# Kernel optimization log

Measured on AMD Instinct MI355X. Metric: run time of the kernel, lower is better.

## Reference

```python
import jax, jax.numpy as jnp
import numpy as np

B, S, H = 4, 2048, 768
NUM_POS = B * (S // 4)  # fixed count of positive clc_label entries (2048, even)
NEG_BIG = -1000000000.0


def setup_inputs() -> dict:
    key = jax.random.key(0)
    k1, k2, k3, k4, k5 = jax.random.split(key, 5)
    encoded_states = jax.random.normal(k1, (B, S, H), dtype=jnp.float32)
    # sorted cell-ids -> contiguous segments for the equality mask
    indicator = jnp.sort(jax.random.randint(k2, (B, S), 0, 256, dtype=jnp.int32), axis=-1)
    # clc_label: first S//4 positions per row are positive targets (class ids in [1,S)),
    # last S//2 positions are -1 (attendable keys), rest 0 (ignored)
    pos_labels = jax.random.randint(k3, (B, S // 4), 1, S, dtype=jnp.int32)
    clc_label = jnp.zeros((B, S), dtype=jnp.int32)
    clc_label = clc_label.at[:, : S // 4].set(pos_labels)
    clc_label = clc_label.at[:, S // 2:].set(-1)
    # uniform_linear params (torch Linear: y = x @ W.T + b)
    W = jax.random.normal(k4, (H, H), dtype=jnp.float32) / np.sqrt(H)
    b = jax.random.normal(k5, (H,), dtype=jnp.float32) * 0.01
    return {"encoded_states": encoded_states, "W": W, "b": b,
            "indicator": indicator, "clc_label": clc_label}


def _ce(logits, labels):
    # mean cross entropy; all labels are > 0 here so ignore_index=0 never triggers
    logp = jax.nn.log_softmax(logits, axis=-1)
    return -jnp.take_along_axis(logp, labels[:, None], axis=1).mean()


def reference(encoded_states, W, b, indicator, clc_label):
    # indicator-equality mask matmul == within-segment sum (the segment-reduce emulation)
    seg_mask = (indicator[:, :, None] == indicator[:, None, :]).astype(encoded_states.dtype)  # [B,S,S]
    agg = jnp.einsum("bij,bjh->bih", seg_mask, encoded_states)  # [B,S,H]
    # Q and K use the SAME linear on the same input -> compute once
    proj = jnp.tanh(agg @ W.T + b)  # [B,S,H]
    scores = jnp.einsum("bih,bjh->bij", proj, proj)  # [B,S,S]
    # attend only to positions where clc_label < 0
    allow = (clc_label < 0)[:, None, :]  # [B,1,S]
    scores = scores + jnp.where(allow, 0.0, NEG_BIG).astype(scores.dtype)
    flat = scores.reshape(-1, S)          # [B*S, S]
    labels = clc_label.reshape(-1)        # [B*S]
    pos_idx = jnp.nonzero(labels > 0, size=NUM_POS)[0]  # row-major order == torch bool-indexing
    logits = flat[pos_idx]                # [NUM_POS, S]
    labs = labels[pos_idx]                # [NUM_POS]
    sep_logits, sep_labels = logits[0::2], labs[0::2]
    tok_logits, tok_labels = logits[1::2], labs[1::2]
    sep_loss = _ce(sep_logits, sep_labels)
    tok_loss = _ce(tok_logits, tok_labels)
    sep_correct = jnp.sum((jnp.argmax(sep_logits, axis=-1).astype(jnp.int32) == sep_labels).astype(jnp.float32))
    tok_correct = jnp.sum((jnp.argmax(tok_logits, axis=-1).astype(jnp.int32) == tok_labels).astype(jnp.float32))
    sep_count = jnp.asarray(sep_logits.shape[0] + 1e-6, dtype=jnp.float32)
    tok_count = jnp.asarray(tok_logits.shape[0] + 1e-6, dtype=jnp.float32)
    return ((sep_loss, sep_correct, sep_count), (tok_loss, tok_correct, tok_count))
```

## Files before the change

### kernel.cpp

```cpp
#include <hip/hip_runtime.h>
#include <math.h>
#include <limits.h>

#define BB 4
#define SS 2048
#define HH 768
#define MAXSEG 256
#define NUM_POS (BB*(SS/4))
#define NEG_BIG -1000000000.0f
#define NSEGSUM (BB*MAXSEG)
#define NWCAST  576

typedef _Float16 f16x8 __attribute__((ext_vector_type(8)));
typedef _Float16 f16x4 __attribute__((ext_vector_type(4)));
typedef float    f32x4 __attribute__((ext_vector_type(4)));

__device__ __forceinline__ int blockExclScan(int v, int* sWave, int lane, int wid)
{
  int x = v;
  #pragma unroll
  for (int off = 1; off < 64; off <<= 1) {
    int y = __shfl_up(x, off, 64);
    if (lane >= off) x += y;
  }
  if (lane == 63) sWave[wid] = x;
  __syncthreads();
  int base = 0;
  for (int w = 0; w < wid; w++) base += sWave[w];
  return base + x - v;
}

__global__ __launch_bounds__(256) void k_front(
    const float* __restrict__ es, const float* __restrict__ W,
    const int* __restrict__ ind, const int* __restrict__ clc,
    _Float16* __restrict__ segsum_h, _Float16* __restrict__ Wh,
    int* __restrict__ seg_id, int* __restrict__ pos_cnt,
    int* __restrict__ allowCnt, int* __restrict__ firstAllow,
    int* __restrict__ posSegOff, int* __restrict__ posSeg,
    float* __restrict__ accum, int* __restrict__ counter)
{
  int t = threadIdx.x;
  int lane = t & 63, wid = t >> 6;
  int blk = blockIdx.x;

  __shared__ int sInd[SS];
  __shared__ int sWave[4];
  __shared__ int sAC[MAXSEG];
  __shared__ int sFA[MAXSEG];
  __shared__ int sStEn[2];

  if (blk >= NSEGSUM + BB) {
    int idx = (blk - NSEGSUM - BB)*256 + t;
    float4 v = ((const float4*)W)[idx];
    f16x4 h;
    h[0] = (_Float16)v.x; h[1] = (_Float16)v.y;
    h[2] = (_Float16)v.z; h[3] = (_Float16)v.w;
    *(f16x4*)(Wh + (size_t)idx*4) = h;
    return;
  }

  if (blk < NSEGSUM) {
    int b = blk >> 8, s = blk & 255;
    for (int i = t; i < SS; i += 256) sInd[i] = ind[b*SS + i];
    if (t == 0) { sStEn[0] = SS; sStEn[1] = SS; }
    __syncthreads();
    int i0 = t * 8;
    int f[8]; int lsum = 0;
    #pragma unroll
    for (int u = 0; u < 8; u++) {
      int i = i0 + u;
      f[u] = (i == 0) ? 0 : (sInd[i] != sInd[i-1]);
      lsum += f[u];
    }
    int run = blockExclScan(lsum, sWave, lane, wid);
    #pragma unroll
    for (int u = 0; u < 8; u++) {
      int i = i0 + u;
      run += f[u];
      if (run == s   && (f[u] || i == 0)) sStEn[0] = i;
      if (run == s+1 && f[u])             sStEn[1] = i;
    }
    __syncthreads();
    int st = sStEn[0], en = sStEn[1];
    float4 acc = {0.f, 0.f, 0.f, 0.f};
    if (t < 192 && st < SS) {
      const float* basep = es + (size_t)b*SS*HH + t*4;
      for (int i = st; i < en; i++) {
        float4 v = *(const float4*)(basep + (size_t)i*HH);
        acc.x += v.x; acc.y += v.y; acc.z += v.z; acc.w += v.w;
      }
    }
    if (t < 192) {
      f16x4 h;
      h[0] = (_Float16)acc.x; h[1] = (_Float16)acc.y;
      h[2] = (_Float16)acc.z; h[3] = (_Float16)acc.w;
      *(f16x4*)(segsum_h + ((size_t)b*MAXSEG + s)*HH + t*4) = h;
    }
    return;
  }

  int b = blk - NSEGSUM;
  if (b == 0 && t < 4) accum[t] = 0.f;
  if (b == 0 && t == 4) *counter = 0;
  for (int i = t; i < SS; i += 256) sInd[i] = ind[b*SS + i];
  sAC[t] = 0; sFA[t] = INT_MAX;
  __syncthreads();

  int i0 = t * 8;
  int f[8], cv[8];
  int lsum = 0;
  #pragma unroll
  for (int u = 0; u < 8; u++) {
    int i = i0 + u;
    f[u] = (i == 0) ? 0 : (sInd[i] != sInd[i-1]);
    cv[u] = clc[b*SS + i];
    lsum += f[u];
  }
  int run = blockExclScan(lsum, sWave, lane, wid);
  int rid[8];
  #pragma unroll
  for (int u = 0; u < 8; u++) {
    run += f[u];
    rid[u] = run;
    seg_id[b*SS + i0 + u] = run;
  }

  #pragma unroll
  for (int u = 0; u < 8; u++) {
    if (cv[u] < 0) {
      atomicAdd(&sAC[rid[u]], 1);
      atomicMin(&sFA[rid[u]], i0 + u);
    }
  }
  __syncthreads();
  allowCnt[b*MAXSEG + t]   = sAC[t];
  firstAllow[b*MAXSEG + t] = sFA[t];
  __syncthreads();

  int p[8], kk[8];
  int psum = 0;
  #pragma unroll
  for (int u = 0; u < 8; u++) { p[u] = (cv[u] > 0) ? 1 : 0; psum += p[u]; }
  int rank = blockExclScan(psum, sWave, lane, wid);
  #pragma unroll
  for (int u = 0; u < 8; u++) {
    kk[u] = rank;
    if (p[u]) rank++;
  }
  if (t == 255) pos_cnt[b] = rank;
  __syncthreads();

  sAC[t] = 0;
  __syncthreads();
  #pragma unroll
  for (int u = 0; u < 8; u++) if (p[u]) atomicAdd(&sAC[rid[u]], 1);
  __syncthreads();
  int cnt = sAC[t];
  int off = blockExclScan(cnt, sWave, lane, wid);
  posSegOff[b*(MAXSEG+1) + t] = off;
  if (t == 255) posSegOff[b*(MAXSEG+1) + 256] = off + cnt;
  __syncthreads();
  sFA[t] = off;
  __syncthreads();
  #pragma unroll
  for (int u = 0; u < 8; u++) {
    if (p[u]) {
      int pos = atomicAdd(&sFA[rid[u]], 1);
      posSeg[b*SS + pos] = (kk[u] << 16) | (i0 + u);
    }
  }
}

__global__ __launch_bounds__(256) void k_gemmU(
    const _Float16* __restrict__ Ah, const _Float16* __restrict__ Wh,
    const float* __restrict__ bias, _Float16* __restrict__ Uh)
{
  int tid = threadIdx.x;
  int w = tid >> 6, lane = tid & 63;
  int tile = blockIdx.x*4 + w;
  int tm = tile / 24, tn = tile % 24;
  int rb = tm*32, cb = tn*32;
  int m0 = lane & 15, quad = lane >> 4;
  const _Float16* A0 = Ah + (size_t)(rb + m0)*HH + quad*8;
  const _Float16* A1 = A0 + (size_t)16*HH;
  const _Float16* B0 = Wh + (size_t)(cb + m0)*HH + quad*8;
  const _Float16* B1 = B0 + (size_t)16*HH;
  f32x4 acc00 = {0.f,0.f,0.f,0.f}, acc01 = {0.f,0.f,0.f,0.f};
  f32x4 acc10 = {0.f,0.f,0.f,0.f}, acc11 = {0.f,0.f,0.f,0.f};
  #pragma unroll 4
  for (int k0 = 0; k0 < HH; k0 += 32) {
    f16x8 a0 = *(const f16x8*)(A0 + k0);
    f16x8 a1 = *(const f16x8*)(A1 + k0);
    f16x8 b0 = *(const f16x8*)(B0 + k0);
    f16x8 b1 = *(const f16x8*)(B1 + k0);
    acc00 = __builtin_amdgcn_mfma_f32_16x16x32_f16(a0, b0, acc00, 0, 0, 0);
    acc01 = __builtin_amdgcn_mfma_f32_16x16x32_f16(a0, b1, acc01, 0, 0, 0);
    acc10 = __builtin_amdgcn_mfma_f32_16x16x32_f16(a1, b0, acc10, 0, 0, 0);
    acc11 = __builtin_amdgcn_mfma_f32_16x16x32_f16(a1, b1, acc11, 0, 0, 0);
  }
  float bc0 = bias[cb + m0], bc1 = bias[cb + 16 + m0];
  int r0 = rb + quad*4;
  #pragma unroll
  for (int i = 0; i < 4; i++) {
    Uh[(size_t)(r0+i)*HH    + cb + m0]      = (_Float16)tanhf(acc00[i] + bc0);
    Uh[(size_t)(r0+i)*HH    + cb + 16 + m0] = (_Float16)tanhf(acc01[i] + bc1);
    Uh[(size_t)(r0+16+i)*HH + cb + m0]      = (_Float16)tanhf(acc10[i] + bc0);
    Uh[(size_t)(r0+16+i)*HH + cb + 16 + m0] = (_Float16)tanhf(acc11[i] + bc1);
  }
}

__global__ __launch_bounds__(256) void k_gramtail(
    const _Float16* __restrict__ Uh, const int* __restrict__ seg_id,
    const int* __restrict__ clc, const int* __restrict__ pos_cnt,
    const int* __restrict__ allowCnt, const int* __restrict__ firstAllow,
    const int* __restrict__ posSegOff, const int* __restrict__ posSeg,
    float* __restrict__ accum, int* __restrict__ counter,
    float* __restrict__ out)
{
  __shared__ float Gs[16][260];
  __shared__ float sP[4][4];
  int t = threadIdx.x;
  int lane = t & 63, wid = t >> 6;
  int b = blockIdx.x >> 4;
  int rb = (blockIdx.x & 15) * 16;
  int m0 = lane & 15, quad = lane >> 4;
  const _Float16* Ub = Uh + (size_t)b*MAXSEG*HH;
  const _Float16* Ap = Ub + (size_t)(rb + m0)*HH + quad*8;

  #pragma unroll
  for (int ct = 0; ct < 4; ct++) {
    int cb = (wid*4 + ct)*16;
    const _Float16* Bp = Ub + (size_t)(cb + m0)*HH + quad*8;
    f32x4 acc = {0.f,0.f,0.f,0.f};
    #pragma unroll 4
    for (int k0 = 0; k0 < HH; k0 += 32) {
      f16x8 a  = *(const f16x8*)(Ap + k0);
      f16x8 bb = *(const f16x8*)(Bp + k0);
      acc = __builtin_amdgcn_mfma_f32_16x16x32_f16(a, bb, acc, 0, 0, 0);
    }
    #pragma unroll
    for (int i = 0; i < 4; i++)
      Gs[quad*4 + i][cb + m0] = acc[i];
  }
  __syncthreads();

  const int* ac = allowCnt + b*MAXSEG;
  const int* fa = firstAllow + b*MAXSEG;
  int base_b = 0;
  for (int x = 0; x < b; x++) base_b += pos_cnt[x];
  float l0 = 0.f, c0 = 0.f, l1 = 0.f, c1 = 0.f;

  #pragma unroll
  for (int q2 = 0; q2 < 4; q2++) {
    int row = wid*4 + q2;
    int si = rb + row;
    float gv[4]; int av[4], fv[4];
    #pragma unroll
    for (int q = 0; q < 4; q++) {
      int s2 = lane + 64*q;
      gv[q] = Gs[row][s2]; av[q] = ac[s2]; fv[q] = fa[s2];
    }
    float m = -INFINITY;
    #pragma unroll
    for (int q = 0; q < 4; q++) if (av[q] > 0) m = fmaxf(m, gv[q]);
    #pragma unroll
    for (int off = 32; off > 0; off >>= 1) m = fmaxf(m, __shfl_xor(m, off, 64));
    float s = 0.f;
    #pragma unroll
    for (int q = 0; q < 4; q++) if (av[q] > 0) s += (float)av[q] * expf(gv[q] - m);
    #pragma unroll
    for (int off = 32; off > 0; off >>= 1) s += __shfl_xor(s, off, 64);
    float bv = -INFINITY; int bi = INT_MAX;
    #pragma unroll
    for (int q = 0; q < 4; q++) {
      if (av[q] > 0 && (gv[q] > bv || (gv[q] == bv && fv[q] < bi))) { bv = gv[q]; bi = fv[q]; }
    }
    #pragma unroll
    for (int off = 32; off > 0; off >>= 1) {
      float ov = __shfl_xor(bv, off, 64);
      int   oi = __shfl_xor(bi, off, 64);
      if (ov > bv || (ov == bv && oi < bi)) { bv = ov; bi = oi; }
    }
    float lseV = m + logf(s);

    int st = posSegOff[b*(MAXSEG+1) + si];
    int en = posSegOff[b*(MAXSEG+1) + si + 1];
    for (int pp = st + lane; pp < en; pp += 64) {
      int e = posSeg[b*SS + pp];
      int i = e & 0xFFFF, k = e >> 16;
      int L = clc[b*SS + i];
      int sL = seg_id[b*SS + L];
      float vL = Gs[row][sL] + (clc[b*SS + L] < 0 ? 0.0f : NEG_BIG);
      float loss = lseV - vL;
      float corr = (bi == L) ? 1.0f : 0.0f;
      if ((base_b + k) & 1) { l1 += loss; c1 += corr; }
      else                  { l0 += loss; c0 += corr; }
    }
  }

  #pragma unroll
  for (int off = 32; off > 0; off >>= 1) {
    l0 += __shfl_down(l0, off, 64);
    c0 += __shfl_down(c0, off, 64);
    l1 += __shfl_down(l1, off, 64);
    c1 += __shfl_down(c1, off, 64);
  }
  if (lane == 0) { sP[wid][0] = l0; sP[wid][1] = c0; sP[wid][2] = l1; sP[wid][3] = c1; }
  __syncthreads();
  if (t == 0) {
    atomicAdd(&accum[0], sP[0][0]+sP[1][0]+sP[2][0]+sP[3][0]);
    atomicAdd(&accum[1], sP[0][1]+sP[1][1]+sP[2][1]+sP[3][1]);
    atomicAdd(&accum[2], sP[0][2]+sP[1][2]+sP[2][2]+sP[3][2]);
    atomicAdd(&accum[3], sP[0][3]+sP[1][3]+sP[2][3]+sP[3][3]);
    __threadfence();
    int old = atomicAdd(counter, 1);
    if (old == (int)gridDim.x - 1) {
      float L0 = atomicAdd(&accum[0], 0.0f);
      float C0 = atomicAdd(&accum[1], 0.0f);
      float L1 = atomicAdd(&accum[2], 0.0f);
      float C1 = atomicAdd(&accum[3], 0.0f);
      float n = (float)(NUM_POS/2);
      out[0] = L0 / n;
      out[1] = C0;
      out[2] = n + 1e-6f;
      out[3] = L1 / n;
      out[4] = C1;
      out[5] = n + 1e-6f;
    }
  }
}

extern "C" void kernel_launch(void* const* d_in, const int* in_sizes, int n_in,
                              void* d_out, int out_size, void* d_ws, size_t ws_size,
                              hipStream_t stream)
{
  const float* es   = (const float*)d_in[0];
  const float* W    = (const float*)d_in[1];
  const float* bias = (const float*)d_in[2];
  const int*   ind  = (const int*)d_in[3];
  const int*   clc  = (const int*)d_in[4];
  float* out = (float*)d_out;

  char* ws = (char*)d_ws;
  float* accum      = (float*)(ws + 0);
  int*   counter    = (int*)(ws + 16);
  int*   pos_cnt    = (int*)(ws + 512);
  int*   seg_id     = (int*)(ws + 8192);
  int*   posSegOff  = (int*)(ws + 40960);
  int*   posSeg     = (int*)(ws + 49152);
  int*   allowCnt   = (int*)(ws + 81920);
  int*   firstAllow = (int*)(ws + 86016);
  _Float16* segsum_h = (_Float16*)(ws + 90112);
  _Float16* Wh       = (_Float16*)(ws + 1662976);
  _Float16* Uh       = (_Float16*)(ws + 2842624);

  k_front<<<NSEGSUM + BB + NWCAST, 256, 0, stream>>>(
      es, W, ind, clc, segsum_h, Wh, seg_id, pos_cnt,
      allowCnt, firstAllow, posSegOff, posSeg, accum, counter);
  k_gemmU<<<192, 256, 0, stream>>>(segsum_h, Wh, bias, Uh);
  k_gramtail<<<64, 256, 0, stream>>>(Uh, seg_id, clc, pos_cnt, allowCnt,
                                     firstAllow, posSegOff, posSeg,
                                     accum, counter, out);
}
```

Baseline: 137.1 us.

## Split fused gram-tail kernel into separate gram and tail kernels for parallelism

Splits the fused Gram-matrix and loss-tail kernel into two launches. The Gram kernel gives each wave one 16x16 tile across 256 blocks and writes the fp32 Gram matrix to workspace. The tail kernel then handles one row per wave across 256 blocks. The aim is to fill more compute units than the former 64-block launch, at the cost of an extra kernel launch and a global-memory round-trip for the Gram matrix.

```diff
diff --git a/kernel.cpp b/kernel.cpp
--- a/kernel.cpp
+++ b/kernel.cpp
@@ -209,93 +209,93 @@
   }
 }
 
-__global__ __launch_bounds__(256) void k_gramtail(
-    const _Float16* __restrict__ Uh, const int* __restrict__ seg_id,
+__global__ __launch_bounds__(256) void k_gram(
+    const _Float16* __restrict__ Uh, float* __restrict__ G)
+{
+  int tid = threadIdx.x;
+  int w = tid >> 6, lane = tid & 63;
+  int tile = blockIdx.x*4 + w;
+  int b = tile >> 8, rem = tile & 255;
+  int rb = (rem >> 4)*16, cb = (rem & 15)*16;
+  int m0 = lane & 15, quad = lane >> 4;
+  const _Float16* Ub = Uh + (size_t)b*MAXSEG*HH;
+  const _Float16* A0 = Ub + (size_t)(rb + m0)*HH + quad*8;
+  const _Float16* B0 = Ub + (size_t)(cb + m0)*HH + quad*8;
+  f32x4 acc = {0.f,0.f,0.f,0.f};
+  #pragma unroll 4
+  for (int k0 = 0; k0 < HH; k0 += 32) {
+    f16x8 a  = *(const f16x8*)(A0 + k0);
+    f16x8 bb = *(const f16x8*)(B0 + k0);
+    acc = __builtin_amdgcn_mfma_f32_16x16x32_f16(a, bb, acc, 0, 0, 0);
+  }
+  float* Gb = G + (size_t)b*MAXSEG*MAXSEG;
+  int r0 = rb + quad*4;
+  #pragma unroll
+  for (int i = 0; i < 4; i++)
+    Gb[(size_t)(r0+i)*MAXSEG + cb + m0] = acc[i];
+}
+
+__global__ __launch_bounds__(256) void k_tail(
+    const float* __restrict__ G, const int* __restrict__ seg_id,
     const int* __restrict__ clc, const int* __restrict__ pos_cnt,
     const int* __restrict__ allowCnt, const int* __restrict__ firstAllow,
     const int* __restrict__ posSegOff, const int* __restrict__ posSeg,
     float* __restrict__ accum, int* __restrict__ counter,
     float* __restrict__ out)
 {
-  __shared__ float Gs[16][260];
   __shared__ float sP[4][4];
   int t = threadIdx.x;
   int lane = t & 63, wid = t >> 6;
-  int b = blockIdx.x >> 4;
-  int rb = (blockIdx.x & 15) * 16;
-  int m0 = lane & 15, quad = lane >> 4;
-  const _Float16* Ub = Uh + (size_t)b*MAXSEG*HH;
-  const _Float16* Ap = Ub + (size_t)(rb + m0)*HH + quad*8;
-
-  #pragma unroll
-  for (int ct = 0; ct < 4; ct++) {
-    int cb = (wid*4 + ct)*16;
-    const _Float16* Bp = Ub + (size_t)(cb + m0)*HH + quad*8;
-    f32x4 acc = {0.f,0.f,0.f,0.f};
-    #pragma unroll 4
-    for (int k0 = 0; k0 < HH; k0 += 32) {
-      f16x8 a  = *(const f16x8*)(Ap + k0);
-      f16x8 bb = *(const f16x8*)(Bp + k0);
-      acc = __builtin_amdgcn_mfma_f32_16x16x32_f16(a, bb, acc, 0, 0, 0);
-    }
-    #pragma unroll
-    for (int i = 0; i < 4; i++)
-      Gs[quad*4 + i][cb + m0] = acc[i];
-  }
-  __syncthreads();
-
+  int row = blockIdx.x * 4 + wid;
+  int b = row >> 8, si = row & 255;
+
+  const float* g = G + ((size_t)b*MAXSEG + si)*MAXSEG;
   const int* ac = allowCnt + b*MAXSEG;
   const int* fa = firstAllow + b*MAXSEG;
+  float gv[4]; int av[4], fv[4];
+  #pragma unroll
+  for (int q = 0; q < 4; q++) {
+    int s2 = lane + 64*q;
+    gv[q] = g[s2]; av[q] = ac[s2]; fv[q] = fa[s2];
+  }
+  float m = -INFINITY;
+  #pragma unroll
+  for (int q = 0; q < 4; q++) if (av[q] > 0) m = fmaxf(m, gv[q]);
+  #pragma unroll
+  for (int off = 32; off > 0; off >>= 1) m = fmaxf(m, __shfl_xor(m, off, 64));
+  float s = 0.f;
+  #pragma unroll
+  for (int q = 0; q < 4; q++) if (av[q] > 0) s += (float)av[q] * expf(gv[q] - m);
+  #pragma unroll
+  for (int off = 32; off > 0; off >>= 1) s += __shfl_xor(s, off, 64);
+  float bv = -INFINITY; int bi = INT_MAX;
+  #pragma unroll
+  for (int q = 0; q < 4; q++) {
+    if (av[q] > 0 && (gv[q] > bv || (gv[q] == bv && fv[q] < bi))) { bv = gv[q]; bi = fv[q]; }
+  }
+  #pragma unroll
+  for (int off = 32; off > 0; off >>= 1) {
+    float ov = __shfl_xor(bv, off, 64);
+    int   oi = __shfl_xor(bi, off, 64);
+    if (ov > bv || (ov == bv && oi < bi)) { bv = ov; bi = oi; }
+  }
+  float lseV = m + logf(s);
+
   int base_b = 0;
   for (int x = 0; x < b; x++) base_b += pos_cnt[x];
+  int st = posSegOff[b*(MAXSEG+1) + si];
+  int en = posSegOff[b*(MAXSEG+1) + si + 1];
   float l0 = 0.f, c0 = 0.f, l1 = 0.f, c1 = 0.f;
-
-  #pragma unroll
-  for (int q2 = 0; q2 < 4; q2++) {
-    int row = wid*4 + q2;
-    int si = rb + row;
-    float gv[4]; int av[4], fv[4];
-    #pragma unroll
-    for (int q = 0; q < 4; q++) {
-      int s2 = lane + 64*q;
-      gv[q] = Gs[row][s2]; av[q] = ac[s2]; fv[q] = fa[s2];
-    }
-    float m = -INFINITY;
-    #pragma unroll
-    for (int q = 0; q < 4; q++) if (av[q] > 0) m = fmaxf(m, gv[q]);
-    #pragma unroll
-    for (int off = 32; off > 0; off >>= 1) m = fmaxf(m, __shfl_xor(m, off, 64));
-    float s = 0.f;
-    #pragma unroll
-    for (int q = 0; q < 4; q++) if (av[q] > 0) s += (float)av[q] * expf(gv[q] - m);
-    #pragma unroll
-    for (int off = 32; off > 0; off >>= 1) s += __shfl_xor(s, off, 64);
-    float bv = -INFINITY; int bi = INT_MAX;
-    #pragma unroll
-    for (int q = 0; q < 4; q++) {
-      if (av[q] > 0 && (gv[q] > bv || (gv[q] == bv && fv[q] < bi))) { bv = gv[q]; bi = fv[q]; }
-    }
-    #pragma unroll
-    for (int off = 32; off > 0; off >>= 1) {
-      float ov = __shfl_xor(bv, off, 64);
-      int   oi = __shfl_xor(bi, off, 64);
-      if (ov > bv || (ov == bv && oi < bi)) { bv = ov; bi = oi; }
-    }
-    float lseV = m + logf(s);
-
-    int st = posSegOff[b*(MAXSEG+1) + si];
-    int en = posSegOff[b*(MAXSEG+1) + si + 1];
-    for (int pp = st + lane; pp < en; pp += 64) {
-      int e = posSeg[b*SS + pp];
-      int i = e & 0xFFFF, k = e >> 16;
-      int L = clc[b*SS + i];
-      int sL = seg_id[b*SS + L];
-      float vL = Gs[row][sL] + (clc[b*SS + L] < 0 ? 0.0f : NEG_BIG);
-      float loss = lseV - vL;
-      float corr = (bi == L) ? 1.0f : 0.0f;
-      if ((base_b + k) & 1) { l1 += loss; c1 += corr; }
-      else                  { l0 += loss; c0 += corr; }
-    }
+  for (int pp = st + lane; pp < en; pp += 64) {
+    int e = posSeg[b*SS + pp];
+    int i = e & 0xFFFF, k = e >> 16;
+    int L = clc[b*SS + i];
+    int sL = seg_id[b*SS + L];
+    float vL = g[sL] + (clc[b*SS + L] < 0 ? 0.0f : NEG_BIG);
+    float loss = lseV - vL;
+    float corr = (bi == L) ? 1.0f : 0.0f;
+    if ((base_b + k) & 1) { l1 += loss; c1 += corr; }
+    else                  { l0 += loss; c0 += corr; }
   }
 
   #pragma unroll
@@ -353,12 +353,14 @@
   _Float16* segsum_h = (_Float16*)(ws + 90112);
   _Float16* Wh       = (_Float16*)(ws + 1662976);
   _Float16* Uh       = (_Float16*)(ws + 2842624);
+  float*    G        = (float*)(ws + 4415488);
 
   k_front<<<NSEGSUM + BB + NWCAST, 256, 0, stream>>>(
       es, W, ind, clc, segsum_h, Wh, seg_id, pos_cnt,
       allowCnt, firstAllow, posSegOff, posSeg, accum, counter);
   k_gemmU<<<192, 256, 0, stream>>>(segsum_h, Wh, bias, Uh);
-  k_gramtail<<<64, 256, 0, stream>>>(Uh, seg_id, clc, pos_cnt, allowCnt,
-                                     firstAllow, posSegOff, posSeg,
-                                     accum, counter, out);
-}
+  k_gram<<<256, 256, 0, stream>>>(Uh, G);
+  k_tail<<<256, 256, 0, stream>>>(G, seg_id, clc, pos_cnt, allowCnt,
+                                  firstAllow, posSegOff, posSeg,
+                                  accum, counter, out);
+}
```

Result: faster. 130.8 us (-4.6%).
